# Performance work log

Hardware: AMD Instinct MI355X
Metric: run time of the kernel (lower is better)

Reference implementation:

```python
import jax, jax.numpy as jnp
import numpy as np

B, S, H = 32, 512, 768          # batch, encoder seq len, hidden size
W, G = 128, 4                   # max words per example, max tokens per word group
NH, HD, FF, NL, NLAB = 4, 192, 2048, 2, 6  # heads, head dim, ffn dim, layers, labels
EPS = 1e-5


def setup_inputs() -> dict:
    key = jax.random.key(0)
    ks = jax.random.split(key, 16)
    s = 0.02
    hidden = jax.random.normal(ks[0], (B, S, H), jnp.float32)
    word_token_idx = jax.random.randint(ks[1], (B, W, G), 0, S).astype(jnp.int32)
    glen = jax.random.randint(ks[2], (B, W), 1, G + 1)
    group_token_mask = jnp.arange(G)[None, None, :] < glen[:, :, None]  # [B,W,G] bool
    nwords = jax.random.randint(ks[3], (B,), W // 2, W + 1)
    word_valid = jnp.arange(W)[None, :] < nwords[:, None]               # [B,W] bool
    return {
        'hidden': hidden,
        'word_token_idx': word_token_idx,
        'group_token_mask': group_token_mask,
        'word_valid': word_valid,
        'qkv_w': jax.random.normal(ks[4], (NL, 3 * H, H), jnp.float32) * s,
        'qkv_b': jnp.zeros((NL, 3 * H), jnp.float32),
        'out_w': jax.random.normal(ks[5], (NL, H, H), jnp.float32) * s,
        'out_b': jnp.zeros((NL, H), jnp.float32),
        'ff1_w': jax.random.normal(ks[6], (NL, FF, H), jnp.float32) * s,
        'ff1_b': jnp.zeros((NL, FF), jnp.float32),
        'ff2_w': jax.random.normal(ks[7], (NL, H, FF), jnp.float32) * s,
        'ff2_b': jnp.zeros((NL, H), jnp.float32),
        'ln1_s': jnp.ones((NL, H), jnp.float32),
        'ln1_b': jnp.zeros((NL, H), jnp.float32),
        'ln2_s': jnp.ones((NL, H), jnp.float32),
        'ln2_b': jnp.zeros((NL, H), jnp.float32),
        'cls_w': jax.random.normal(ks[8], (NLAB, H), jnp.float32) * s,
        'cls_b': jnp.zeros((NLAB,), jnp.float32),
    }


def _ln(x, s, b):
    m = x.mean(-1, keepdims=True)
    v = ((x - m) ** 2).mean(-1, keepdims=True)
    return (x - m) * jax.lax.rsqrt(v + EPS) * s + b


def reference(hidden, word_token_idx, group_token_mask, word_valid,
              qkv_w, qkv_b, out_w, out_b, ff1_w, ff1_b, ff2_w, ff2_b,
              ln1_s, ln1_b, ln2_s, ln2_b, cls_w, cls_b):
    dt = hidden.dtype
    # ragged per-word gather + masked mean over each subword group: [B,W,G,H]
    gathered = jax.vmap(lambda h, i: h[i])(hidden, word_token_idx)
    gm = group_token_mask[..., None].astype(dt)
    wemb = (gathered * gm).sum(2) / jnp.maximum(gm.sum(2), 1.0)   # [B,W,H]
    # invalid (padded) words are zero, matching torch pad_sequence zero-padding
    wemb = wemb * word_valid[..., None].astype(dt)
    cls = hidden[:, 0, :]
    x = jnp.concatenate([cls[:, None, :], wemb], axis=1)          # [B, W+1, H]
    # key padding mask: True = padded position; CLS slot always valid
    pad = jnp.concatenate([jnp.zeros((B, 1), bool), ~word_valid], axis=1)
    neg = jnp.finfo(dt).min
    Lw = W + 1
    scale = 1.0 / np.sqrt(HD)
    for l in range(NL):  # 2 post-norm TransformerEncoder layers
        qkv = x @ qkv_w[l].T + qkv_b[l]
        q, k, v = jnp.split(qkv, 3, axis=-1)
        q = q.reshape(B, Lw, NH, HD).transpose(0, 2, 1, 3)
        k = k.reshape(B, Lw, NH, HD).transpose(0, 2, 1, 3)
        v = v.reshape(B, Lw, NH, HD).transpose(0, 2, 1, 3)
        scores = jnp.einsum('bhqd,bhkd->bhqk', q, k) * scale
        scores = jnp.where(pad[:, None, None, :], neg, scores)
        a = jax.nn.softmax(scores, axis=-1)
        ctx = jnp.einsum('bhqk,bhkd->bhqd', a, v).transpose(0, 2, 1, 3).reshape(B, Lw, H)
        attn = ctx @ out_w[l].T + out_b[l]
        x = _ln(x + attn, ln1_s[l], ln1_b[l])
        h1 = jax.nn.relu(x @ ff1_w[l].T + ff1_b[l])
        x = _ln(x + h1 @ ff2_w[l].T + ff2_b[l], ln2_s[l], ln2_b[l])
    pooled = x[:, 0, :]
    logits = pooled @ cls_w.T + cls_b
    return (logits, pooled)
```

## Files before the change

### kernel.cpp

```cpp
#include <hip/hip_runtime.h>
#include <hip/hip_bf16.h>
#include <math.h>

#define B_  32
#define S_  512
#define H_  768
#define W_  128
#define G_  4
#define LW  129
#define NH_ 4
#define HD_ 192
#define FF_ 2048
#define NL_ 2
#define NLAB_ 6
#define M_   (B_ * LW)
#define MPAD 4224
#define EPS_ 1e-5f
#define SCALE_ 0.07216878364870323f

#define TP 192
#define KP 160
#define KR 144
#define KLD 200

#define QW_SZ (3 * H_ * H_)
#define OW_SZ (H_ * H_)
#define F1_SZ (FF_ * H_)
#define F2_SZ (H_ * FF_)
#define WL_SZ (QW_SZ + OW_SZ + F1_SZ + F2_SZ)

typedef __bf16 bf16_8 __attribute__((ext_vector_type(8)));
typedef float  f32x4  __attribute__((ext_vector_type(4)));
typedef unsigned short ushort8_t __attribute__((ext_vector_type(8)));

__device__ __forceinline__ float b2f(unsigned short u) {
    union { unsigned int i; float f; } c; c.i = ((unsigned int)u) << 16; return c.f;
}
__device__ __forceinline__ unsigned short f2b(float f) {
    union { float f; unsigned int u; } c; c.f = f;
    unsigned int u = c.u;
    return (unsigned short)((u + 0x7FFFu + ((u >> 16) & 1u)) >> 16);
}

__device__ __forceinline__ float wave_sum(float v) {
#pragma unroll
    for (int off = 1; off < 64; off <<= 1) v += __shfl_xor(v, off, 64);
    return v;
}
__device__ __forceinline__ float block_sum(float v, float* red) {
    v = wave_sum(v);
    int wid = threadIdx.x >> 6, lane = threadIdx.x & 63;
    if (lane == 0) red[wid] = v;
    __syncthreads();
    float r = (red[0] + red[1]) + (red[2] + red[3]);
    __syncthreads();
    return r;
}

__global__ __launch_bounds__(256) void build_x_kernel(
    const float* __restrict__ hidden,
    const int*   __restrict__ wti,
    const int*   __restrict__ gmask,
    const int*   __restrict__ wvalid,
    float* __restrict__ x,
    unsigned short* __restrict__ xb)
{
    int t = blockIdx.x;
    int b = blockIdx.y;
    int tid = threadIdx.x;
    size_t xo = ((size_t)b * LW + t) * H_;
    if (t == 0) {
        const float* src = hidden + (size_t)b * S_ * H_;
#pragma unroll
        for (int i = 0; i < 3; i++) {
            float v = src[tid + i * 256];
            x[xo + tid + i * 256] = v;
            xb[xo + tid + i * 256] = f2b(v);
        }
    } else {
        int w = t - 1;
        int valid = wvalid[b * W_ + w];
        int ids[G_]; float msk[G_]; float cnt = 0.f;
#pragma unroll
        for (int g = 0; g < G_; g++) {
            ids[g] = wti[(b * W_ + w) * G_ + g];
            msk[g] = (gmask[(b * W_ + w) * G_ + g] != 0) ? 1.f : 0.f;
            cnt += msk[g];
        }
        float inv = valid ? (1.f / fmaxf(cnt, 1.f)) : 0.f;
#pragma unroll
        for (int i = 0; i < 3; i++) {
            int c = tid + i * 256;
            float a = 0.f;
#pragma unroll
            for (int g = 0; g < G_; g++)
                a += msk[g] * hidden[((size_t)b * S_ + ids[g]) * H_ + c];
            float v = a * inv;
            x[xo + c] = v;
            xb[xo + c] = f2b(v);
        }
    }
}

__global__ __launch_bounds__(256) void zero_pad_xb(unsigned short* __restrict__ xb) {
    int i = blockIdx.x * 256 + threadIdx.x;
    if (i < (MPAD - M_) * H_) xb[(size_t)M_ * H_ + i] = 0;
}

__global__ __launch_bounds__(256) void cvt_layer_kernel(
    const float4* __restrict__ qw, const float4* __restrict__ ow,
    const float4* __restrict__ f1, const float4* __restrict__ f2,
    ushort4* __restrict__ dst)
{
    int i = blockIdx.x * 256 + threadIdx.x;
    float4 v;
    if (i < QW_SZ / 4)                          v = qw[i];
    else if (i < (QW_SZ + OW_SZ) / 4)           v = ow[i - QW_SZ / 4];
    else if (i < (QW_SZ + OW_SZ + F1_SZ) / 4)   v = f1[i - (QW_SZ + OW_SZ) / 4];
    else                                        v = f2[i - (QW_SZ + OW_SZ + F1_SZ) / 4];
    ushort4 o; o.x = f2b(v.x); o.y = f2b(v.y); o.z = f2b(v.z); o.w = f2b(v.w);
    dst[i] = o;
}

template <int BM, int BN, int BK, int RELU, int OUTBF, int SWZ>
__global__ __launch_bounds__(256) void gemm_mfma(
    const unsigned short* __restrict__ A,
    const unsigned short* __restrict__ Bw,
    const float* __restrict__ bias,
    void* __restrict__ Cout,
    int N, int K)
{
    constexpr int MI  = BM / 32;
    constexpr int NJ  = BN / 32;
    constexpr int CPR = BK / 8;
    constexpr int RPL = 2048 / BK;
    constexpr int SA  = BM * BK / 2048;
    constexpr int SB  = BN * BK / 2048;

    __shared__ __align__(16) unsigned short As[BM * BK];
    __shared__ __align__(16) unsigned short Bs[BN * BK];

    const int tid  = threadIdx.x;
    const int lane = tid & 63;
    const int wid  = tid >> 6;

    int bx = blockIdx.x, by = blockIdx.y;
    if (SWZ) {
        int nx = gridDim.x;
        int total = nx * gridDim.y;
        int id = by * nx + bx;
        int id2 = (id & 7) * (total >> 3) + (id >> 3);
        by = id2 / nx; bx = id2 - by * nx;
    }
    const int bm = by * BM;
    const int bn = bx * BN;

    const int wm = (wid & 1) * (BM / 2);
    const int wn = (wid >> 1) * (BN / 2);
    const int r  = lane & 15;
    const int q8 = lane >> 4;
    const int m8 = r & (CPR - 1);

    const int srow = tid / CPR;
    const int scol = (tid % CPR) ^ (srow & (CPR - 1));
    const unsigned short* Ag = A  + (size_t)(bm + srow) * K + scol * 8;
    const unsigned short* Bg = Bw + (size_t)(bn + srow) * K + scol * 8;

    const bf16_8* Af = (const bf16_8*)As;
    const bf16_8* Bf = (const bf16_8*)Bs;
    int arow[MI], brow[NJ];
#pragma unroll
    for (int i = 0; i < MI; i++) arow[i] = (wm + i * 16 + r) * CPR;
#pragma unroll
    for (int j = 0; j < NJ; j++) brow[j] = (wn + j * 16 + r) * CPR;

    f32x4 acc[MI][NJ];
#pragma unroll
    for (int i = 0; i < MI; i++)
#pragma unroll
        for (int j = 0; j < NJ; j++) acc[i][j] = (f32x4){0.f, 0.f, 0.f, 0.f};

    for (int k0 = 0; k0 < K; k0 += BK) {
#pragma unroll
        for (int s = 0; s < SA; s++)
            __builtin_amdgcn_global_load_lds(
                (const __attribute__((address_space(1))) void*)(Ag + (size_t)(s * RPL) * K + k0),
                (__attribute__((address_space(3))) void*)(As + s * 2048 + tid * 8), 16, 0, 0);
#pragma unroll
        for (int s = 0; s < SB; s++)
            __builtin_amdgcn_global_load_lds(
                (const __attribute__((address_space(1))) void*)(Bg + (size_t)(s * RPL) * K + k0),
                (__attribute__((address_space(3))) void*)(Bs + s * 2048 + tid * 8), 16, 0, 0);
        __syncthreads();
#pragma unroll
        for (int ks = 0; ks < BK / 32; ks++) {
            const int cc = (ks * 4 + q8) ^ m8;
            bf16_8 a[MI], b[NJ];
#pragma unroll
            for (int i = 0; i < MI; i++) a[i] = Af[arow[i] + cc];
#pragma unroll
            for (int j = 0; j < NJ; j++) b[j] = Bf[brow[j] + cc];
#pragma unroll
            for (int i = 0; i < MI; i++)
#pragma unroll
                for (int j = 0; j < NJ; j++)
                    acc[i][j] = __builtin_amdgcn_mfma_f32_16x16x32_bf16(a[i], b[j], acc[i][j], 0, 0, 0);
        }
        __syncthreads();
    }

    int col[NJ]; float bv[NJ];
#pragma unroll
    for (int j = 0; j < NJ; j++) { col[j] = bn + wn + j * 16 + r; bv[j] = bias[col[j]]; }
    const int row0 = bm + wm + ((lane >> 4) << 2);
#pragma unroll
    for (int i = 0; i < MI; i++) {
#pragma unroll
        for (int rg = 0; rg < 4; rg++) {
            size_t rowoff = (size_t)(row0 + i * 16 + rg) * N;
#pragma unroll
            for (int j = 0; j < NJ; j++) {
                float v = acc[i][j][rg] + bv[j];
                if (RELU) v = fmaxf(v, 0.f);
                if (OUTBF) ((unsigned short*)Cout)[rowoff + col[j]] = f2b(v);
                else       ((float*)Cout)[rowoff + col[j]] = v;
            }
        }
    }
}

__global__ __launch_bounds__(256) void vt_kernel(
    const unsigned short* __restrict__ qkv,
    unsigned short* __restrict__ vtb)
{
    __shared__ __align__(16) unsigned short Vs[KR * KLD];
    int bh = blockIdx.x;
    int b = bh >> 2, h = bh & 3;
    int tid = threadIdx.x;
    for (int c = tid; c < KR * 24; c += 256) {
        int t = c / 24, j = c - t * 24;
        ushort8_t v = (ushort8_t){0,0,0,0,0,0,0,0};
        if (t < LW)
            v = *(const ushort8_t*)(qkv + (size_t)(b * LW + t) * (3 * H_) + 2 * H_ + h * HD_ + j * 8);
        *(ushort8_t*)(&Vs[t * KLD + j * 8]) = v;
    }
    __syncthreads();
    size_t obase = (size_t)bh * (HD_ * KP);
    for (int c = tid; c < HD_ * (KP / 4); c += 256) {
        int d = c / (KP / 4), t0 = (c - d * (KP / 4)) * 4;
        ushort4 o;
        o.x = (t0 + 0 < KR) ? Vs[(t0 + 0) * KLD + d] : 0;
        o.y = (t0 + 1 < KR) ? Vs[(t0 + 1) * KLD + d] : 0;
        o.z = (t0 + 2 < KR) ? Vs[(t0 + 2) * KLD + d] : 0;
        o.w = (t0 + 3 < KR) ? Vs[(t0 + 3) * KLD + d] : 0;
        *(ushort4*)(&vtb[obase + (size_t)d * KP + t0]) = o;
    }
}

__global__ __launch_bounds__(256) void attn_score_kernel(
    const unsigned short* __restrict__ qkv,
    const int*            __restrict__ wvalid,
    unsigned short*       __restrict__ pb)
{
    __shared__ __align__(16) unsigned short Ks[KR * KLD];
    __shared__ float msk[KR];
    int mb = blockIdx.x;
    int bh = blockIdx.y;
    int b = bh >> 2, h = bh & 3;
    int tid = threadIdx.x, lane = tid & 63, wid = tid >> 6;
    int q = lane >> 4, r = lane & 15;

    for (int c = tid; c < KR * 24; c += 256) {
        int t = c / 24, j = c - t * 24;
        ushort8_t v = (ushort8_t){0,0,0,0,0,0,0,0};
        if (t < LW)
            v = *(const ushort8_t*)(qkv + (size_t)(b * LW + t) * (3 * H_) + H_ + h * HD_ + j * 8);
        *(ushort8_t*)(&Ks[t * KLD + j * 8]) = v;
    }
    if (tid < KR) {
        bool valid = (tid == 0) || (tid <= W_ && wvalid[b * W_ + tid - 1] != 0);
        msk[tid] = valid ? 0.f : -1e30f;
    }
    __syncthreads();

    const int qrow0 = mb * 64 + wid * 16;
    const unsigned short* Qp = qkv + ((size_t)(b * LW) + qrow0 + r) * (3 * H_) + h * HD_;

    f32x4 acc[9];
#pragma unroll
    for (int nt = 0; nt < 9; nt++) acc[nt] = (f32x4){0.f, 0.f, 0.f, 0.f};

    for (int ks = 0; ks < HD_ / 32; ks++) {
        bf16_8 a = *(const bf16_8*)(Qp + ks * 32 + q * 8);
#pragma unroll
        for (int nt = 0; nt < 9; nt++) {
            bf16_8 bfrag = *(const bf16_8*)(&Ks[(nt * 16 + r) * KLD + ks * 32 + q * 8]);
            acc[nt] = __builtin_amdgcn_mfma_f32_16x16x32_bf16(a, bfrag, acc[nt], 0, 0, 0);
        }
    }

    float mk[9];
#pragma unroll
    for (int nt = 0; nt < 9; nt++) mk[nt] = msk[nt * 16 + r];

    size_t pbase = (size_t)bh * (TP * KP);
#pragma unroll
    for (int rg = 0; rg < 4; rg++) {
        float v[9]; float mx = -1e30f;
#pragma unroll
        for (int nt = 0; nt < 9; nt++) { v[nt] = acc[nt][rg] * SCALE_ + mk[nt]; mx = fmaxf(mx, v[nt]); }
#pragma unroll
        for (int off = 1; off < 16; off <<= 1) mx = fmaxf(mx, __shfl_xor(mx, off, 64));
        float s = 0.f;
#pragma unroll
        for (int nt = 0; nt < 9; nt++) { v[nt] = __expf(v[nt] - mx); s += v[nt]; }
#pragma unroll
        for (int off = 1; off < 16; off <<= 1) s += __shfl_xor(s, off, 64);
        float inv = 1.f / s;
        int row = qrow0 + q * 4 + rg;
#pragma unroll
        for (int nt = 0; nt < 9; nt++)
            pb[pbase + (size_t)row * KP + nt * 16 + r] = f2b(v[nt] * inv);
        pb[pbase + (size_t)row * KP + KR + r] = 0;
    }
}

__global__ __launch_bounds__(256) void attn_pv_kernel(
    const unsigned short* __restrict__ pb,
    const unsigned short* __restrict__ vtb,
    unsigned short*       __restrict__ ctx)
{
    int mb = blockIdx.x;
    int bh = blockIdx.y;
    int b = bh >> 2, h = bh & 3;
    int tid = threadIdx.x, lane = tid & 63, wid = tid >> 6;
    int q = lane >> 4, r = lane & 15;
    int wm = (wid & 1) * 32, wn = (wid >> 1) * 96;

    size_t pbase = (size_t)bh * (TP * KP);
    size_t vbase = (size_t)bh * (HD_ * KP);

    f32x4 acc[2][6];
#pragma unroll
    for (int i = 0; i < 2; i++)
#pragma unroll
        for (int j = 0; j < 6; j++) acc[i][j] = (f32x4){0.f, 0.f, 0.f, 0.f};

    for (int ks = 0; ks < KP / 32; ks++) {
        bf16_8 a[2], bb[6];
#pragma unroll
        for (int i = 0; i < 2; i++)
            a[i] = *(const bf16_8*)(pb + pbase + (size_t)(mb * 64 + wm + i * 16 + r) * KP + ks * 32 + q * 8);
#pragma unroll
        for (int j = 0; j < 6; j++)
            bb[j] = *(const bf16_8*)(vtb + vbase + (size_t)(wn + j * 16 + r) * KP + ks * 32 + q * 8);
#pragma unroll
        for (int i = 0; i < 2; i++)
#pragma unroll
            for (int j = 0; j < 6; j++)
                acc[i][j] = __builtin_amdgcn_mfma_f32_16x16x32_bf16(a[i], bb[j], acc[i][j], 0, 0, 0);
    }

#pragma unroll
    for (int i = 0; i < 2; i++) {
#pragma unroll
        for (int rg = 0; rg < 4; rg++) {
            int t = mb * 64 + wm + i * 16 + q * 4 + rg;
            if (t < LW) {
                size_t rowoff = (size_t)(b * LW + t) * H_ + h * HD_;
#pragma unroll
                for (int j = 0; j < 6; j++)
                    ctx[rowoff + wn + j * 16 + r] = f2b(acc[i][j][rg]);
            }
        }
    }
}

__global__ __launch_bounds__(256) void add_ln_kernel(
    float* __restrict__ x, const float* __restrict__ res,
    const float* __restrict__ sc, const float* __restrict__ bi,
    unsigned short* __restrict__ xb)
{
    __shared__ float red[4];
    int row = blockIdx.x;
    int tid = threadIdx.x;
    size_t base = (size_t)row * H_;
    float v[3];
    float sum = 0.f;
#pragma unroll
    for (int i = 0; i < 3; i++) {
        int c = tid + i * 256;
        float t = x[base + c] + res[base + c];
        v[i] = t; sum += t;
    }
    sum = block_sum(sum, red);
    float mean = sum * (1.f / H_);
    float var = 0.f;
#pragma unroll
    for (int i = 0; i < 3; i++) { float d = v[i] - mean; var += d * d; }
    var = block_sum(var, red);
    float inv = rsqrtf(var * (1.f / H_) + EPS_);
#pragma unroll
    for (int i = 0; i < 3; i++) {
        int c = tid + i * 256;
        float r = (v[i] - mean) * inv * sc[c] + bi[c];
        x[base + c] = r;
        xb[base + c] = f2b(r);
    }
}

__global__ __launch_bounds__(384) void cls_kernel(
    const float* __restrict__ x,
    const float* __restrict__ cls_w, const float* __restrict__ cls_b,
    float* __restrict__ out)
{
    int b = blockIdx.x;
    int tid = threadIdx.x;
    const float* p = &x[((size_t)b * LW) * H_];
    for (int c = tid; c < H_; c += 384) out[B_ * NLAB_ + b * H_ + c] = p[c];
    int w = tid >> 6, lane = tid & 63;
    if (w < NLAB_) {
        const float* wv = &cls_w[w * H_];
        float acc = 0.f;
#pragma unroll
        for (int i = 0; i < H_ / 64; i++) {
            int c = lane + i * 64;
            acc += p[c] * wv[c];
        }
        acc = wave_sum(acc);
        if (lane == 0) out[b * NLAB_ + w] = acc + cls_b[w];
    }
}

extern "C" void kernel_launch(void* const* d_in, const int* in_sizes, int n_in,
                              void* d_out, int out_size, void* d_ws, size_t ws_size,
                              hipStream_t stream) {
    const float* hidden = (const float*)d_in[0];
    const int*   wti    = (const int*)d_in[1];
    const int*   gmask  = (const int*)d_in[2];
    const int*   wvalid = (const int*)d_in[3];
    const float* qkv_w  = (const float*)d_in[4];
    const float* qkv_b  = (const float*)d_in[5];
    const float* out_w  = (const float*)d_in[6];
    const float* out_b  = (const float*)d_in[7];
    const float* ff1_w  = (const float*)d_in[8];
    const float* ff1_b  = (const float*)d_in[9];
    const float* ff2_w  = (const float*)d_in[10];
    const float* ff2_b  = (const float*)d_in[11];
    const float* ln1_s  = (const float*)d_in[12];
    const float* ln1_b  = (const float*)d_in[13];
    const float* ln2_s  = (const float*)d_in[14];
    const float* ln2_b  = (const float*)d_in[15];
    const float* cls_w  = (const float*)d_in[16];
    const float* cls_b  = (const float*)d_in[17];
    float* out = (float*)d_out;

    const size_t XSZ = (size_t)MPAD * H_;
    const size_t ASZ = (size_t)128 * TP * KP;
    float* x32   = (float*)d_ws;
    float* tmp32 = x32 + XSZ;
    unsigned short* vtb = (unsigned short*)tmp32;
    unsigned short* pb  = vtb + ASZ;
    unsigned short* xb   = (unsigned short*)(tmp32 + ASZ);
    unsigned short* ctxb = xb + XSZ;
    unsigned short* qkvb = ctxb + XSZ;
    unsigned short* wb   = qkvb + (size_t)MPAD * 3 * H_;

    build_x_kernel<<<dim3(LW, B_), 256, 0, stream>>>(hidden, wti, gmask, wvalid, x32, xb);
    zero_pad_xb<<<288, 256, 0, stream>>>(xb);

    const int GM = MPAD / 64;
    for (int l = 0; l < NL_; l++) {
        cvt_layer_kernel<<<WL_SZ / 4 / 256, 256, 0, stream>>>(
            (const float4*)(qkv_w + (size_t)l * QW_SZ), (const float4*)(out_w + (size_t)l * OW_SZ),
            (const float4*)(ff1_w + (size_t)l * F1_SZ), (const float4*)(ff2_w + (size_t)l * F2_SZ),
            (ushort4*)wb);
        gemm_mfma<64, 128, 64, 0, 1, 0><<<dim3(3 * H_ / 128, GM), 256, 0, stream>>>(
            xb, wb, qkv_b + (size_t)l * 3 * H_, qkvb, 3 * H_, H_);
        vt_kernel<<<128, 256, 0, stream>>>(qkvb, vtb);
        attn_score_kernel<<<dim3(3, 128), 256, 0, stream>>>(qkvb, wvalid, pb);
        attn_pv_kernel<<<dim3(3, 128), 256, 0, stream>>>(pb, vtb, ctxb);
        gemm_mfma<64, 64, 64, 0, 0, 1><<<dim3(H_ / 64, GM), 256, 0, stream>>>(
            ctxb, wb + QW_SZ, out_b + (size_t)l * H_, tmp32, H_, H_);
        add_ln_kernel<<<M_, 256, 0, stream>>>(x32, tmp32,
            ln1_s + (size_t)l * H_, ln1_b + (size_t)l * H_, xb);
        gemm_mfma<64, 128, 64, 1, 1, 1><<<dim3(FF_ / 128, GM), 256, 0, stream>>>(
            xb, wb + QW_SZ + OW_SZ, ff1_b + (size_t)l * FF_, qkvb, FF_, H_);
        gemm_mfma<64, 64, 64, 0, 0, 1><<<dim3(H_ / 64, GM), 256, 0, stream>>>(
            qkvb, wb + QW_SZ + OW_SZ + F1_SZ, ff2_b + (size_t)l * H_, tmp32, H_, FF_);
        add_ln_kernel<<<M_, 256, 0, stream>>>(x32, tmp32,
            ln2_s + (size_t)l * H_, ln2_b + (size_t)l * H_, xb);
    }
    cls_kernel<<<B_, 384, 0, stream>>>(x32, cls_w, cls_b, out);
    (void)in_sizes; (void)n_in; (void)out_size; (void)ws_size;
}
```

Measured before the change: 444.4 us.

## Drop fp32 residual stream, keep activations in bf16, convert weights once

Removes the fp32 copy of the residual stream x and the fp32 GEMM outputs. The out-proj and FF2 GEMMs now write bf16, and add-LN reads and writes only bf16. Weights for both layers are converted in a single launch before the loop, and pad-row zeroing is folded into build_x, which saves launches. The aim is to cut memory traffic and launch count, at the cost of precision, since the residual path and final pooled output are now rounded to bf16. The larger weight buffer must also fit in the workspace.

```diff
diff --git a/kernel.cpp b/kernel.cpp
--- a/kernel.cpp
+++ b/kernel.cpp
@@ -62,21 +62,23 @@
     const int*   __restrict__ wti,
     const int*   __restrict__ gmask,
     const int*   __restrict__ wvalid,
-    float* __restrict__ x,
     unsigned short* __restrict__ xb)
 {
     int t = blockIdx.x;
     int b = blockIdx.y;
     int tid = threadIdx.x;
+    if (t >= LW) {
+        int pr = M_ + b * 3 + (t - LW);
+        size_t xo = (size_t)pr * H_;
+#pragma unroll
+        for (int i = 0; i < 3; i++) xb[xo + tid + i * 256] = 0;
+        return;
+    }
     size_t xo = ((size_t)b * LW + t) * H_;
     if (t == 0) {
         const float* src = hidden + (size_t)b * S_ * H_;
 #pragma unroll
-        for (int i = 0; i < 3; i++) {
-            float v = src[tid + i * 256];
-            x[xo + tid + i * 256] = v;
-            xb[xo + tid + i * 256] = f2b(v);
-        }
+        for (int i = 0; i < 3; i++) xb[xo + tid + i * 256] = f2b(src[tid + i * 256]);
     } else {
         int w = t - 1;
         int valid = wvalid[b * W_ + w];
@@ -95,29 +97,25 @@
 #pragma unroll
             for (int g = 0; g < G_; g++)
                 a += msk[g] * hidden[((size_t)b * S_ + ids[g]) * H_ + c];
-            float v = a * inv;
-            x[xo + c] = v;
-            xb[xo + c] = f2b(v);
-        }
-    }
-}
-
-__global__ __launch_bounds__(256) void zero_pad_xb(unsigned short* __restrict__ xb) {
-    int i = blockIdx.x * 256 + threadIdx.x;
-    if (i < (MPAD - M_) * H_) xb[(size_t)M_ * H_ + i] = 0;
-}
-
-__global__ __launch_bounds__(256) void cvt_layer_kernel(
+            xb[xo + c] = f2b(a * inv);
+        }
+    }
+}
+
+__global__ __launch_bounds__(256) void cvt_all_kernel(
     const float4* __restrict__ qw, const float4* __restrict__ ow,
     const float4* __restrict__ f1, const float4* __restrict__ f2,
     ushort4* __restrict__ dst)
 {
+    constexpr int WL4 = WL_SZ / 4;
     int i = blockIdx.x * 256 + threadIdx.x;
+    int l = (i < WL4) ? 0 : 1;
+    int j = i - l * WL4;
     float4 v;
-    if (i < QW_SZ / 4)                          v = qw[i];
-    else if (i < (QW_SZ + OW_SZ) / 4)           v = ow[i - QW_SZ / 4];
-    else if (i < (QW_SZ + OW_SZ + F1_SZ) / 4)   v = f1[i - (QW_SZ + OW_SZ) / 4];
-    else                                        v = f2[i - (QW_SZ + OW_SZ + F1_SZ) / 4];
+    if (j < QW_SZ / 4)                          v = qw[l * (QW_SZ / 4) + j];
+    else if (j < (QW_SZ + OW_SZ) / 4)           v = ow[l * (OW_SZ / 4) + j - QW_SZ / 4];
+    else if (j < (QW_SZ + OW_SZ + F1_SZ) / 4)   v = f1[l * (F1_SZ / 4) + j - (QW_SZ + OW_SZ) / 4];
+    else                                        v = f2[l * (F2_SZ / 4) + j - (QW_SZ + OW_SZ + F1_SZ) / 4];
     ushort4 o; o.x = f2b(v.x); o.y = f2b(v.y); o.z = f2b(v.z); o.w = f2b(v.w);
     dst[i] = o;
 }
@@ -377,9 +375,8 @@
 }
 
 __global__ __launch_bounds__(256) void add_ln_kernel(
-    float* __restrict__ x, const float* __restrict__ res,
-    const float* __restrict__ sc, const float* __restrict__ bi,
-    unsigned short* __restrict__ xb)
+    unsigned short* __restrict__ xb, const unsigned short* __restrict__ res,
+    const float* __restrict__ sc, const float* __restrict__ bi)
 {
     __shared__ float red[4];
     int row = blockIdx.x;
@@ -390,7 +387,7 @@
 #pragma unroll
     for (int i = 0; i < 3; i++) {
         int c = tid + i * 256;
-        float t = x[base + c] + res[base + c];
+        float t = b2f(xb[base + c]) + b2f(res[base + c]);
         v[i] = t; sum += t;
     }
     sum = block_sum(sum, red);
@@ -403,21 +400,19 @@
 #pragma unroll
     for (int i = 0; i < 3; i++) {
         int c = tid + i * 256;
-        float r = (v[i] - mean) * inv * sc[c] + bi[c];
-        x[base + c] = r;
-        xb[base + c] = f2b(r);
+        xb[base + c] = f2b((v[i] - mean) * inv * sc[c] + bi[c]);
     }
 }
 
 __global__ __launch_bounds__(384) void cls_kernel(
-    const float* __restrict__ x,
+    const unsigned short* __restrict__ xb,
     const float* __restrict__ cls_w, const float* __restrict__ cls_b,
     float* __restrict__ out)
 {
     int b = blockIdx.x;
     int tid = threadIdx.x;
-    const float* p = &x[((size_t)b * LW) * H_];
-    for (int c = tid; c < H_; c += 384) out[B_ * NLAB_ + b * H_ + c] = p[c];
+    const unsigned short* p = &xb[((size_t)b * LW) * H_];
+    for (int c = tid; c < H_; c += 384) out[B_ * NLAB_ + b * H_ + c] = b2f(p[c]);
     int w = tid >> 6, lane = tid & 63;
     if (w < NLAB_) {
         const float* wv = &cls_w[w * H_];
@@ -425,7 +420,7 @@
 #pragma unroll
         for (int i = 0; i < H_ / 64; i++) {
             int c = lane + i * 64;
-            acc += p[c] * wv[c];
+            acc += b2f(p[c]) * wv[c];
         }
         acc = wave_sum(acc);
         if (lane == 0) out[b * NLAB_ + w] = acc + cls_b[w];
@@ -457,40 +452,39 @@
 
     const size_t XSZ = (size_t)MPAD * H_;
     const size_t ASZ = (size_t)128 * TP * KP;
-    float* x32   = (float*)d_ws;
-    float* tmp32 = x32 + XSZ;
-    unsigned short* vtb = (unsigned short*)tmp32;
-    unsigned short* pb  = vtb + ASZ;
-    unsigned short* xb   = (unsigned short*)(tmp32 + ASZ);
+    unsigned short* U    = (unsigned short*)d_ws;
+    unsigned short* vtb  = U;
+    unsigned short* pb   = U + ASZ;
+    unsigned short* tmpb = U;
+    unsigned short* xb   = U + 2 * ASZ;
     unsigned short* ctxb = xb + XSZ;
     unsigned short* qkvb = ctxb + XSZ;
     unsigned short* wb   = qkvb + (size_t)MPAD * 3 * H_;
 
-    build_x_kernel<<<dim3(LW, B_), 256, 0, stream>>>(hidden, wti, gmask, wvalid, x32, xb);
-    zero_pad_xb<<<288, 256, 0, stream>>>(xb);
+    build_x_kernel<<<dim3(LW + 3, B_), 256, 0, stream>>>(hidden, wti, gmask, wvalid, xb);
+    cvt_all_kernel<<<2 * WL_SZ / 4 / 256, 256, 0, stream>>>(
+        (const float4*)qkv_w, (const float4*)out_w,
+        (const float4*)ff1_w, (const float4*)ff2_w, (ushort4*)wb);
 
     const int GM = MPAD / 64;
     for (int l = 0; l < NL_; l++) {
-        cvt_layer_kernel<<<WL_SZ / 4 / 256, 256, 0, stream>>>(
-            (const float4*)(qkv_w + (size_t)l * QW_SZ), (const float4*)(out_w + (size_t)l * OW_SZ),
-            (const float4*)(ff1_w + (size_t)l * F1_SZ), (const float4*)(ff2_w + (size_t)l * F2_SZ),
-            (ushort4*)wb);
+        unsigned short* wbl = wb + (size_t)l * WL_SZ;
         gemm_mfma<64, 128, 64, 0, 1, 0><<<dim3(3 * H_ / 128, GM), 256, 0, stream>>>(
-            xb, wb, qkv_b + (size_t)l * 3 * H_, qkvb, 3 * H_, H_);
+            xb, wbl, qkv_b + (size_t)l * 3 * H_, qkvb, 3 * H_, H_);
         vt_kernel<<<128, 256, 0, stream>>>(qkvb, vtb);
         attn_score_kernel<<<dim3(3, 128), 256, 0, stream>>>(qkvb, wvalid, pb);
         attn_pv_kernel<<<dim3(3, 128), 256, 0, stream>>>(pb, vtb, ctxb);
-        gemm_mfma<64, 64, 64, 0, 0, 1><<<dim3(H_ / 64, GM), 256, 0, stream>>>(
-            ctxb, wb + QW_SZ, out_b + (size_t)l * H_, tmp32, H_, H_);
-        add_ln_kernel<<<M_, 256, 0, stream>>>(x32, tmp32,
-            ln1_s + (size_t)l * H_, ln1_b + (size_t)l * H_, xb);
+        gemm_mfma<64, 64, 64, 0, 1, 1><<<dim3(H_ / 64, GM), 256, 0, stream>>>(
+            ctxb, wbl + QW_SZ, out_b + (size_t)l * H_, tmpb, H_, H_);
+        add_ln_kernel<<<M_, 256, 0, stream>>>(xb, tmpb,
+            ln1_s + (size_t)l * H_, ln1_b + (size_t)l * H_);
         gemm_mfma<64, 128, 64, 1, 1, 1><<<dim3(FF_ / 128, GM), 256, 0, stream>>>(
-            xb, wb + QW_SZ + OW_SZ, ff1_b + (size_t)l * FF_, qkvb, FF_, H_);
-        gemm_mfma<64, 64, 64, 0, 0, 1><<<dim3(H_ / 64, GM), 256, 0, stream>>>(
-            qkvb, wb + QW_SZ + OW_SZ + F1_SZ, ff2_b + (size_t)l * H_, tmp32, H_, FF_);
-        add_ln_kernel<<<M_, 256, 0, stream>>>(x32, tmp32,
-            ln2_s + (size_t)l * H_, ln2_b + (size_t)l * H_, xb);
-    }
-    cls_kernel<<<B_, 384, 0, stream>>>(x32, cls_w, cls_b, out);
+            xb, wbl + QW_SZ + OW_SZ, ff1_b + (size_t)l * FF_, qkvb, FF_, H_);
+        gemm_mfma<64, 64, 64, 0, 1, 1><<<dim3(H_ / 64, GM), 256, 0, stream>>>(
+            qkvb, wbl + QW_SZ + OW_SZ + F1_SZ, ff2_b + (size_t)l * H_, tmpb, H_, FF_);
+        add_ln_kernel<<<M_, 256, 0, stream>>>(xb, tmpb,
+            ln2_s + (size_t)l * H_, ln2_b + (size_t)l * H_);
+    }
+    cls_kernel<<<B_, 384, 0, stream>>>(xb, cls_w, cls_b, out);
     (void)in_sizes; (void)n_in; (void)out_size; (void)ws_size;
 }
```

After: 419.1 us. -5.7%, faster.
